# Performance work log

Hardware: AMD Instinct MI355X
Metric: run time of the kernel (lower is better)

The kernel has to match this reference:

```python
import jax, jax.numpy as jnp
import numpy as np

N = 50000      # nodes
E = 800000     # edges (avg degree 16)
D = 128        # hidden dim
L = 3          # message-passing layers
NU = 1         # DRew nu -> delay = max(k - nu, 0)


def setup_inputs() -> dict:
    key = jax.random.key(0)
    ks = jax.random.split(key, 6)
    x = jax.random.normal(ks[0], (N, D), dtype=jnp.float32)
    edge_index = jax.random.randint(ks[1], (2, E), 0, N)          # [2, E] (src, dst)
    edge_attr = jax.random.randint(ks[2], (E,), 1, L + 1)          # edge types in {1..L}
    scale = 1.0 / np.sqrt(D).astype(np.float32)
    Ws = jax.random.normal(ks[3], (L, D, D), dtype=jnp.float32) * scale       # mlp_s per layer
    bs = jnp.zeros((L, D), dtype=jnp.float32)
    Wk = jax.random.normal(ks[4], (L, L, D, D), dtype=jnp.float32) * scale    # mlp_k, padded; layer t uses k=1..t+1
    bk = jnp.zeros((L, L, D), dtype=jnp.float32)
    eps = jnp.zeros((L,), dtype=jnp.float32)
    return dict(x=x, edge_index=edge_index, edge_attr=edge_attr,
                Ws=Ws, bs=bs, Wk=Wk, bk=bk, eps=eps)


def reference(x, edge_index, edge_attr, Ws, bs, Wk, bk, eps):
    src, dst = edge_index[0], edge_index[1]
    xs = [x]
    for t in range(L):
        xt = xs[-1]
        # out = (1 + eps) * mlp_s(x)
        out = (1.0 + eps[t]) * jax.nn.relu(xt @ Ws[t] + bs[t])
        for k in range(1, t + 2):
            delay = max(k - NU, 0)
            x_src = xs[t - delay]                       # delayed node features
            mask = (edge_attr == k).astype(xt.dtype)    # edge-type mask (replaces boolean column select)
            msg = x_src[src] * mask[:, None]            # gather + mask: [E, D]
            agg = jax.ops.segment_sum(msg, dst, num_segments=N)  # scatter-add per destination
            out = out + jax.nn.relu(agg @ Wk[t, k - 1] + bk[t, k - 1])  # mlp_k(k)
        # gin_nn_post is an empty Sequential -> identity; then F.relu; then residual
        h = jax.nn.relu(out)
        xs.append(xt + h)
    return xs[-1]
```

## Files before the change

kernel.cpp:

```cpp
#include <hip/hip_runtime.h>
#include <hip/hip_bf16.h>


#define NODES 50000
#define EDGES 800000
#define DIM   128
#define ND    ((long)NODES * DIM)
#define NB3   (3 * NODES)
#define NPART 8
#define PSIZE (NODES / NPART)
#define NROWP 50048
#define NBLKS ((NB3 + 255) / 256)
#define NCELL 192
#define SORTN (NCELL * NBLKS)

typedef __attribute__((ext_vector_type(8))) short  bf16x8;
typedef __attribute__((ext_vector_type(4))) float  f32x4;

#define LDS_STRIDE 136

__global__ __launch_bounds__(256) void convw_kernel(
    const float* __restrict__ Ws, const float* __restrict__ Wk,
    __hip_bfloat16* __restrict__ WT) {
  int m = blockIdx.x;
  const float* src = (m < 3) ? (Ws + (long)m * 16384) : (Wk + (long)(m - 3) * 16384);
  __hip_bfloat16* dst = WT + (long)m * 16384;
  for (int idx = threadIdx.x; idx < 16384; idx += 256) {
    int k = idx >> 7, n = idx & 127;
    dst[n * 128 + k] = __float2bfloat16(src[idx]);
  }
}

__global__ __launch_bounds__(256) void x2b_kernel(
    const float4* __restrict__ xin, uint2* __restrict__ xbo, long n4) {
  long i = (long)blockIdx.x * 256 + threadIdx.x;
  if (i >= n4) return;
  float4 v = xin[i];
  union { __hip_bfloat16 h[4]; uint2 u; } pk;
  pk.h[0] = __float2bfloat16(v.x); pk.h[1] = __float2bfloat16(v.y);
  pk.h[2] = __float2bfloat16(v.z); pk.h[3] = __float2bfloat16(v.w);
  xbo[i] = pk.u;
}

__global__ __launch_bounds__(256) void zrow_kernel(
    __hip_bfloat16* __restrict__ xb0, __hip_bfloat16* __restrict__ xb1,
    __hip_bfloat16* __restrict__ xb2) {
  int i = threadIdx.x;
  if (i < DIM) {
    xb0[(long)NODES * DIM + i] = __float2bfloat16(0.f);
    xb1[(long)NODES * DIM + i] = __float2bfloat16(0.f);
    xb2[(long)NODES * DIM + i] = __float2bfloat16(0.f);
  }
}

__global__ __launch_bounds__(256) void hist_kernel(
    const int* __restrict__ ei, const int* __restrict__ attr,
    int* __restrict__ counts, int E) {
  int e = blockIdx.x * 256 + threadIdx.x;
  if (e >= E) return;
  atomicAdd(&counts[ei[E + e] * 3 + (attr[e] - 1)], 1);
}

__global__ __launch_bounds__(256) void scan_a_kernel(
    const int* __restrict__ counts, int* __restrict__ partial,
    int* __restrict__ blocksums, int n) {
  __shared__ int tmp[256];
  int gid = blockIdx.x * 256 + threadIdx.x;
  int v = (gid < n) ? ((counts[gid] + 3) & ~3) : 0;
  tmp[threadIdx.x] = v;
  __syncthreads();
  for (int off = 1; off < 256; off <<= 1) {
    int t = (threadIdx.x >= off) ? tmp[threadIdx.x - off] : 0;
    __syncthreads();
    tmp[threadIdx.x] += t;
    __syncthreads();
  }
  if (gid < n) partial[gid] = tmp[threadIdx.x] - v;
  if (threadIdx.x == 255) blocksums[blockIdx.x] = tmp[255];
}

__global__ __launch_bounds__(256) void scan_b_kernel(int* __restrict__ bs, int nb) {
  __shared__ int tmp[256];
  __shared__ int carry;
  if (threadIdx.x == 0) carry = 0;
  __syncthreads();
  for (int base = 0; base < nb; base += 256) {
    int gid = base + threadIdx.x;
    int v = (gid < nb) ? bs[gid] : 0;
    tmp[threadIdx.x] = v;
    __syncthreads();
    for (int off = 1; off < 256; off <<= 1) {
      int t = (threadIdx.x >= off) ? tmp[threadIdx.x - off] : 0;
      __syncthreads();
      tmp[threadIdx.x] += t;
      __syncthreads();
    }
    if (gid < nb) bs[gid] = tmp[threadIdx.x] - v + carry;
    __syncthreads();
    if (threadIdx.x == 0) carry += tmp[255];
    __syncthreads();
  }
}

__global__ __launch_bounds__(256) void scan_c_kernel(
    int* __restrict__ rowptr, int* __restrict__ cursor,
    const int* __restrict__ bs, int* __restrict__ csr, int n) {
  int gid = blockIdx.x * 256 + threadIdx.x;
  if (gid >= n) return;
  int cnt = cursor[gid];
  int pcnt = (cnt + 3) & ~3;
  int val = rowptr[gid] + bs[blockIdx.x];
  rowptr[gid] = val;
  cursor[gid] = val;
  for (int i = cnt; i < pcnt; ++i) csr[val + i] = NODES;
  if (gid == n - 1) rowptr[n] = val + pcnt;
}

__global__ __launch_bounds__(256) void fill_kernel(
    const int* __restrict__ ei, const int* __restrict__ attr,
    int* __restrict__ cursor, int* __restrict__ csr_src, int E) {
  int p = blockIdx.x & (NPART - 1);
  int chunk = blockIdx.x >> 3;
  int e = chunk * 256 + threadIdx.x;
  if (e >= E) return;
  int d = ei[E + e];
  int lo = p * PSIZE;
  if (d < lo || d >= lo + PSIZE) return;
  int pos = atomicAdd(&cursor[d * 3 + (attr[e] - 1)], 1);
  csr_src[pos] = ei[e];
}

__device__ __forceinline__ int bucket_cell(const int* rowptr, int b) {
  int c = (rowptr[b + 1] - rowptr[b]) >> 2;
  if (c > 63) c = 63;
  int km1 = b - (b / 3) * 3;
  return km1 * 64 + (63 - c);
}

__global__ __launch_bounds__(256) void bhist_kernel(
    const int* __restrict__ rowptr, int* __restrict__ G) {
  __shared__ int h[NCELL];
  if (threadIdx.x < NCELL) h[threadIdx.x] = 0;
  __syncthreads();
  int b = blockIdx.x * 256 + threadIdx.x;
  if (b < NB3) atomicAdd(&h[bucket_cell(rowptr, b)], 1);
  __syncthreads();
  if (threadIdx.x < NCELL) G[threadIdx.x * NBLKS + blockIdx.x] = h[threadIdx.x];
}

__global__ __launch_bounds__(256) void fscan_a_kernel(
    const int* __restrict__ in, int* __restrict__ partial,
    int* __restrict__ blocksums, int n) {
  __shared__ int tmp[256];
  int gid = blockIdx.x * 256 + threadIdx.x;
  int v = (gid < n) ? in[gid] : 0;
  tmp[threadIdx.x] = v;
  __syncthreads();
  for (int off = 1; off < 256; off <<= 1) {
    int t = (threadIdx.x >= off) ? tmp[threadIdx.x - off] : 0;
    __syncthreads();
    tmp[threadIdx.x] += t;
    __syncthreads();
  }
  if (gid < n) partial[gid] = tmp[threadIdx.x] - v;
  if (threadIdx.x == 255) blocksums[blockIdx.x] = tmp[255];
}

__global__ __launch_bounds__(256) void fscan_c_kernel(
    int* __restrict__ partial, const int* __restrict__ bs, int n) {
  int gid = blockIdx.x * 256 + threadIdx.x;
  if (gid >= n) return;
  partial[gid] += bs[blockIdx.x];
}

__global__ __launch_bounds__(256) void bfill_kernel(
    const int* __restrict__ rowptr, const int* __restrict__ Gscan,
    int* __restrict__ wl) {
  __shared__ int base[NCELL];
  if (threadIdx.x < NCELL)
    base[threadIdx.x] = Gscan[threadIdx.x * NBLKS + blockIdx.x];
  __syncthreads();
  int b = blockIdx.x * 256 + threadIdx.x;
  if (b >= NB3) return;
  int pos = atomicAdd(&base[bucket_cell(rowptr, b)], 1);
  wl[pos] = b;
}

__global__ __launch_bounds__(256, 6) void gather_kernel(
    const __hip_bfloat16* __restrict__ s0,
    const __hip_bfloat16* __restrict__ s1,
    const __hip_bfloat16* __restrict__ s2,
    const int* __restrict__ rowptr, const int* __restrict__ csr,
    const int* __restrict__ wl,
    __hip_bfloat16* __restrict__ ag0, __hip_bfloat16* __restrict__ ag1,
    __hip_bfloat16* __restrict__ ag2, int nwork) {
  int group = (blockIdx.x * 256 + threadIdx.x) >> 4;
  int lane16 = threadIdx.x & 15;
  if (group >= nwork) return;
  int b = wl[group];
  int d = b / 3;
  int km1 = b - d * 3;
  const __hip_bfloat16* xb = (km1 == 0) ? s0 : ((km1 == 1) ? s1 : s2);
  __hip_bfloat16* ag = (km1 == 0) ? ag0 : ((km1 == 1) ? ag1 : ag2);
  int beg = rowptr[b], end = rowptr[b + 1];
  float a0 = 0.f, a1 = 0.f, a2 = 0.f, a3 = 0.f,
        a4 = 0.f, a5 = 0.f, a6 = 0.f, a7 = 0.f;
  for (int base = beg; base < end; base += 16) {
    int idxv = csr[base + lane16];
    int cnt = end - base; if (cnt > 16) cnt = 16;
    for (int j = 0; j < cnt; j += 4) {
      int q0 = __shfl(idxv, j + 0, 16);
      int q1 = __shfl(idxv, j + 1, 16);
      int q2 = __shfl(idxv, j + 2, 16);
      int q3 = __shfl(idxv, j + 3, 16);
      uint4 v0 = *(const uint4*)(xb + (long)q0 * DIM + lane16 * 8);
      uint4 v1 = *(const uint4*)(xb + (long)q1 * DIM + lane16 * 8);
      uint4 v2 = *(const uint4*)(xb + (long)q2 * DIM + lane16 * 8);
      uint4 v3 = *(const uint4*)(xb + (long)q3 * DIM + lane16 * 8);
      a0 += __uint_as_float(v0.x << 16) + __uint_as_float(v1.x << 16)
          + __uint_as_float(v2.x << 16) + __uint_as_float(v3.x << 16);
      a1 += __uint_as_float(v0.x & 0xffff0000u) + __uint_as_float(v1.x & 0xffff0000u)
          + __uint_as_float(v2.x & 0xffff0000u) + __uint_as_float(v3.x & 0xffff0000u);
      a2 += __uint_as_float(v0.y << 16) + __uint_as_float(v1.y << 16)
          + __uint_as_float(v2.y << 16) + __uint_as_float(v3.y << 16);
      a3 += __uint_as_float(v0.y & 0xffff0000u) + __uint_as_float(v1.y & 0xffff0000u)
          + __uint_as_float(v2.y & 0xffff0000u) + __uint_as_float(v3.y & 0xffff0000u);
      a4 += __uint_as_float(v0.z << 16) + __uint_as_float(v1.z << 16)
          + __uint_as_float(v2.z << 16) + __uint_as_float(v3.z << 16);
      a5 += __uint_as_float(v0.z & 0xffff0000u) + __uint_as_float(v1.z & 0xffff0000u)
          + __uint_as_float(v2.z & 0xffff0000u) + __uint_as_float(v3.z & 0xffff0000u);
      a6 += __uint_as_float(v0.w << 16) + __uint_as_float(v1.w << 16)
          + __uint_as_float(v2.w << 16) + __uint_as_float(v3.w << 16);
      a7 += __uint_as_float(v0.w & 0xffff0000u) + __uint_as_float(v1.w & 0xffff0000u)
          + __uint_as_float(v2.w & 0xffff0000u) + __uint_as_float(v3.w & 0xffff0000u);
    }
  }
  union { __hip_bfloat16 h[8]; uint4 u; } pk;
  pk.h[0] = __float2bfloat16(a0); pk.h[1] = __float2bfloat16(a1);
  pk.h[2] = __float2bfloat16(a2); pk.h[3] = __float2bfloat16(a3);
  pk.h[4] = __float2bfloat16(a4); pk.h[5] = __float2bfloat16(a5);
  pk.h[6] = __float2bfloat16(a6); pk.h[7] = __float2bfloat16(a7);
  *(uint4*)(ag + (long)d * DIM + lane16 * 8) = pk.u;
}

__global__ __launch_bounds__(256, 4) void lgemm_kernel(
    const float* __restrict__ xt,
    const __hip_bfloat16* __restrict__ xbSelf,
    const __hip_bfloat16* __restrict__ ag0,
    const __hip_bfloat16* __restrict__ ag1,
    const __hip_bfloat16* __restrict__ ag2,
    const __hip_bfloat16* __restrict__ WT,
    const float* __restrict__ bs_t,
    const float* __restrict__ bk_t,
    const float* __restrict__ epsp,
    float* __restrict__ xn,
    __hip_bfloat16* __restrict__ xnb,
    int t) {
  __shared__ __hip_bfloat16 b_lds[128 * LDS_STRIDE];

  int tid = threadIdx.x;
  long row0 = (long)blockIdx.x * 64;
  int wave = tid >> 6, lane = tid & 63;
  int l15 = lane & 15, q = lane >> 4;
  long arow = row0 + wave * 16 + l15;

  const __hip_bfloat16* Asrc[4] = {xbSelf, ag0, ag1, ag2};
  f32x4 out[8];

  for (int p = 0; p <= t + 1; ++p) {
    if (p > 0) __syncthreads();
    const __hip_bfloat16* Am = Asrc[p];
    uint4 af[4];
#pragma unroll
    for (int k0i = 0; k0i < 4; ++k0i)
      af[k0i] = *(const uint4*)(Am + arow * DIM + k0i * 32 + 8 * q);
    const __hip_bfloat16* W = (p == 0) ? (WT + (long)t * 16384)
                                       : (WT + (long)(3 + t * 3 + (p - 1)) * 16384);
    {
      const uint4* bq = (const uint4*)W;
#pragma unroll
      for (int i = 0; i < 8; ++i) {
        int idx = tid + 256 * i;
        int n = idx >> 4, k8 = idx & 15;
        uint4 v = bq[idx];
        *(uint4*)(b_lds + n * LDS_STRIDE + k8 * 8) = v;
      }
    }
    __syncthreads();

    f32x4 acc[8] = {};
#pragma unroll
    for (int k0i = 0; k0i < 4; ++k0i) {
      bf16x8 a = __builtin_bit_cast(bf16x8, af[k0i]);
#pragma unroll
      for (int j = 0; j < 8; ++j) {
        bf16x8 bfr = *(const bf16x8*)(b_lds + (16 * j + l15) * LDS_STRIDE + k0i * 32 + 8 * q);
        acc[j] = __builtin_amdgcn_mfma_f32_16x16x32_bf16(a, bfr, acc[j], 0, 0, 0);
      }
    }
    if (p == 0) {
      float sc = 1.0f + *epsp;
#pragma unroll
      for (int j = 0; j < 8; ++j) {
        float b = bs_t[16 * j + l15];
#pragma unroll
        for (int r = 0; r < 4; ++r) out[j][r] = sc * fmaxf(acc[j][r] + b, 0.f);
      }
    } else {
      const float* bb = bk_t + (p - 1) * 128;
#pragma unroll
      for (int j = 0; j < 8; ++j) {
        float b = bb[16 * j + l15];
#pragma unroll
        for (int r = 0; r < 4; ++r) out[j][r] += fmaxf(acc[j][r] + b, 0.f);
      }
    }
  }

  long rbase = row0 + wave * 16 + q * 4;
#pragma unroll
  for (int j = 0; j < 8; ++j) {
    int col = 16 * j + l15;
#pragma unroll
    for (int r = 0; r < 4; ++r) {
      long grow = rbase + r;
      if (grow < NODES) {
        float v = xt[grow * DIM + col] + fmaxf(out[j][r], 0.f);
        xn[grow * DIM + col] = v;
        xnb[grow * DIM + col] = __float2bfloat16(v);
      }
    }
  }
}

extern "C" void kernel_launch(void* const* d_in, const int* in_sizes, int n_in,
                              void* d_out, int out_size, void* d_ws, size_t ws_size,
                              hipStream_t stream) {
  const float* x    = (const float*)d_in[0];
  const int*   ei   = (const int*)d_in[1];
  const int*   attr = (const int*)d_in[2];
  const float* Ws   = (const float*)d_in[3];
  const float* bs   = (const float*)d_in[4];
  const float* Wk   = (const float*)d_in[5];
  const float* bk   = (const float*)d_in[6];
  const float* eps  = (const float*)d_in[7];
  float* out = (float*)d_out;

  char* ws = (char*)d_ws;
  size_t off = 0;
  auto alloc = [&](size_t bytes) { char* p = ws + off; off += (bytes + 255) & ~(size_t)255; return p; };
  const size_t ROWB = (size_t)NROWP * DIM * 2;
  float* xs1 = (float*)alloc(ND * 4);
  float* xs2 = (float*)alloc(ND * 4);
  __hip_bfloat16* xb0 = (__hip_bfloat16*)alloc(ROWB);
  __hip_bfloat16* xb1 = (__hip_bfloat16*)alloc(ROWB);
  __hip_bfloat16* xb2 = (__hip_bfloat16*)alloc(ROWB);
  __hip_bfloat16* xb3 = (__hip_bfloat16*)alloc(ROWB);
  __hip_bfloat16* ag0 = (__hip_bfloat16*)alloc(ROWB);
  __hip_bfloat16* ag1 = (__hip_bfloat16*)alloc(ROWB);
  __hip_bfloat16* ag2 = (__hip_bfloat16*)alloc(ROWB);
  __hip_bfloat16* WT  = (__hip_bfloat16*)alloc(12 * 16384 * 2);
  int* cursor    = (int*)alloc((size_t)NB3 * 4);
  int* rowptr    = (int*)alloc((size_t)(NB3 + 1) * 4);
  int* blocksums = (int*)alloc(1024 * 4);
  int* G         = (int*)alloc((size_t)SORTN * 4);
  int* bsum2     = (int*)alloc(1024 * 4);
  int* wl        = (int*)alloc((size_t)NB3 * 4);
  int* csr_src   = (int*)alloc((size_t)(EDGES + 4 * NB3 + 16) * 4);

  hipLaunchKernelGGL(convw_kernel, dim3(12), dim3(256), 0, stream, Ws, Wk, WT);
  hipLaunchKernelGGL(x2b_kernel, dim3((int)(ND / 4 / 256)), dim3(256), 0, stream,
                     (const float4*)x, (uint2*)xb0, ND / 4);
  hipLaunchKernelGGL(zrow_kernel, dim3(1), dim3(256), 0, stream, xb0, xb1, xb2);
  hipMemsetAsync(cursor, 0, (size_t)NB3 * 4, stream);
  int egrid  = (EDGES + 255) / 256;
  int sgridA = (NB3 + 255) / 256;
  hipLaunchKernelGGL(hist_kernel, dim3(egrid), dim3(256), 0, stream, ei, attr, cursor, EDGES);
  hipLaunchKernelGGL(scan_a_kernel, dim3(sgridA), dim3(256), 0, stream, cursor, rowptr, blocksums, NB3);
  hipLaunchKernelGGL(scan_b_kernel, dim3(1), dim3(256), 0, stream, blocksums, sgridA);
  hipLaunchKernelGGL(scan_c_kernel, dim3(sgridA), dim3(256), 0, stream, rowptr, cursor, blocksums, csr_src, NB3);
  hipLaunchKernelGGL(fill_kernel, dim3(egrid * NPART), dim3(256), 0, stream, ei, attr, cursor, csr_src, EDGES);

  int fgrid = (SORTN + 255) / 256;
  hipLaunchKernelGGL(bhist_kernel, dim3(NBLKS), dim3(256), 0, stream, rowptr, G);
  hipLaunchKernelGGL(fscan_a_kernel, dim3(fgrid), dim3(256), 0, stream, G, G, bsum2, SORTN);
  hipLaunchKernelGGL(scan_b_kernel, dim3(1), dim3(256), 0, stream, bsum2, fgrid);
  hipLaunchKernelGGL(fscan_c_kernel, dim3(fgrid), dim3(256), 0, stream, G, bsum2, SORTN);
  hipLaunchKernelGGL(bfill_kernel, dim3(NBLKS), dim3(256), 0, stream, rowptr, G, wl);

  int ggrid = (NODES + 63) / 64;
  auto glaunch = [&](int nwork, const __hip_bfloat16* s0, const __hip_bfloat16* s1,
                     const __hip_bfloat16* s2) {
    int blocks = (nwork * 16 + 255) / 256;
    hipLaunchKernelGGL(gather_kernel, dim3(blocks), dim3(256), 0, stream,
                       s0, s1, s2, rowptr, csr_src, wl, ag0, ag1, ag2, nwork);
  };

  glaunch(NODES, xb0, nullptr, nullptr);
  hipLaunchKernelGGL(lgemm_kernel, dim3(ggrid), dim3(256), 0, stream,
                     x, xb0, ag0, ag1, ag2, WT, bs + 0, bk + 0, eps + 0, xs1, xb1, 0);
  glaunch(2 * NODES, xb1, xb0, nullptr);
  hipLaunchKernelGGL(lgemm_kernel, dim3(ggrid), dim3(256), 0, stream,
                     xs1, xb1, ag0, ag1, ag2, WT, bs + 128, bk + 3 * 128, eps + 1, xs2, xb2, 1);
  glaunch(3 * NODES, xb2, xb1, xb0);
  hipLaunchKernelGGL(lgemm_kernel, dim3(ggrid), dim3(256), 0, stream,
                     xs2, xb2, ag0, ag1, ag2, WT, bs + 256, bk + 6 * 128, eps + 2, out, xb3, 2);
}
```

Baseline: 358.5 us.

## Fuse setup kernels and keep residual stream in bf16 only

Merges weight conversion, x-to-bf16 conversion, zero-row writes and the cursor memset into one init kernel. Folds the bucket histogram into the scan-finalize kernel and the final scan add into bfill, cutting several launches. The lgemm epilogue now reads the residual from the bf16 copy and writes only bf16 for intermediate layers, writing fp32 only at the end. This drops fp32 residual reads and writes but accumulates the residual path in bf16, which loses precision.

```diff
diff --git a/kernel.cpp b/kernel.cpp
--- a/kernel.cpp
+++ b/kernel.cpp
@@ -19,37 +19,36 @@
 
 #define LDS_STRIDE 136
 
-__global__ __launch_bounds__(256) void convw_kernel(
-    const float* __restrict__ Ws, const float* __restrict__ Wk,
-    __hip_bfloat16* __restrict__ WT) {
-  int m = blockIdx.x;
-  const float* src = (m < 3) ? (Ws + (long)m * 16384) : (Wk + (long)(m - 3) * 16384);
-  __hip_bfloat16* dst = WT + (long)m * 16384;
-  for (int idx = threadIdx.x; idx < 16384; idx += 256) {
-    int k = idx >> 7, n = idx & 127;
-    dst[n * 128 + k] = __float2bfloat16(src[idx]);
-  }
-}
-
-__global__ __launch_bounds__(256) void x2b_kernel(
-    const float4* __restrict__ xin, uint2* __restrict__ xbo, long n4) {
-  long i = (long)blockIdx.x * 256 + threadIdx.x;
-  if (i >= n4) return;
-  float4 v = xin[i];
-  union { __hip_bfloat16 h[4]; uint2 u; } pk;
-  pk.h[0] = __float2bfloat16(v.x); pk.h[1] = __float2bfloat16(v.y);
-  pk.h[2] = __float2bfloat16(v.z); pk.h[3] = __float2bfloat16(v.w);
-  xbo[i] = pk.u;
-}
-
-__global__ __launch_bounds__(256) void zrow_kernel(
-    __hip_bfloat16* __restrict__ xb0, __hip_bfloat16* __restrict__ xb1,
-    __hip_bfloat16* __restrict__ xb2) {
-  int i = threadIdx.x;
-  if (i < DIM) {
-    xb0[(long)NODES * DIM + i] = __float2bfloat16(0.f);
-    xb1[(long)NODES * DIM + i] = __float2bfloat16(0.f);
-    xb2[(long)NODES * DIM + i] = __float2bfloat16(0.f);
+__global__ __launch_bounds__(256) void init_kernel(
+    const float* __restrict__ x, const float* __restrict__ Ws,
+    const float* __restrict__ Wk, __hip_bfloat16* __restrict__ xb0,
+    __hip_bfloat16* __restrict__ xb1, __hip_bfloat16* __restrict__ xb2,
+    __hip_bfloat16* __restrict__ WT, int* __restrict__ cursor) {
+  int b = blockIdx.x, tid = threadIdx.x;
+  long i = (long)b * 256 + tid;
+  if (i < ND / 4) {
+    float4 v = ((const float4*)x)[i];
+    union { __hip_bfloat16 h[4]; uint2 u; } pk;
+    pk.h[0] = __float2bfloat16(v.x); pk.h[1] = __float2bfloat16(v.y);
+    pk.h[2] = __float2bfloat16(v.z); pk.h[3] = __float2bfloat16(v.w);
+    ((uint2*)xb0)[i] = pk.u;
+  }
+  if (b < 12) {
+    const float* src = (b < 3) ? (Ws + (long)b * 16384) : (Wk + (long)(b - 3) * 16384);
+    __hip_bfloat16* dst = WT + (long)b * 16384;
+    for (int idx = tid; idx < 16384; idx += 256) {
+      int k = idx >> 7, n = idx & 127;
+      dst[n * 128 + k] = __float2bfloat16(src[idx]);
+    }
+  }
+  if (b >= 12 && b < 12 + NBLKS) {
+    int g = (b - 12) * 256 + tid;
+    if (g < NB3) cursor[g] = 0;
+  }
+  if (b == 599 && tid < DIM) {
+    xb0[(long)NODES * DIM + tid] = __float2bfloat16(0.f);
+    xb1[(long)NODES * DIM + tid] = __float2bfloat16(0.f);
+    xb2[(long)NODES * DIM + tid] = __float2bfloat16(0.f);
   }
 }
 
@@ -102,18 +101,28 @@
   }
 }
 
-__global__ __launch_bounds__(256) void scan_c_kernel(
+__global__ __launch_bounds__(256) void scanc_bhist_kernel(
     int* __restrict__ rowptr, int* __restrict__ cursor,
-    const int* __restrict__ bs, int* __restrict__ csr, int n) {
+    const int* __restrict__ bs, int* __restrict__ csr,
+    int* __restrict__ G, int n) {
+  __shared__ int h[NCELL];
+  if (threadIdx.x < NCELL) h[threadIdx.x] = 0;
+  __syncthreads();
   int gid = blockIdx.x * 256 + threadIdx.x;
-  if (gid >= n) return;
-  int cnt = cursor[gid];
-  int pcnt = (cnt + 3) & ~3;
-  int val = rowptr[gid] + bs[blockIdx.x];
-  rowptr[gid] = val;
-  cursor[gid] = val;
-  for (int i = cnt; i < pcnt; ++i) csr[val + i] = NODES;
-  if (gid == n - 1) rowptr[n] = val + pcnt;
+  if (gid < n) {
+    int cnt = cursor[gid];
+    int pcnt = (cnt + 3) & ~3;
+    int val = rowptr[gid] + bs[blockIdx.x];
+    rowptr[gid] = val;
+    cursor[gid] = val;
+    for (int i = cnt; i < pcnt; ++i) csr[val + i] = NODES;
+    if (gid == n - 1) rowptr[n] = val + pcnt;
+    int c = pcnt >> 2; if (c > 63) c = 63;
+    int km1 = gid - (gid / 3) * 3;
+    atomicAdd(&h[km1 * 64 + (63 - c)], 1);
+  }
+  __syncthreads();
+  if (threadIdx.x < NCELL) G[threadIdx.x * NBLKS + blockIdx.x] = h[threadIdx.x];
 }
 
 __global__ __launch_bounds__(256) void fill_kernel(
@@ -130,24 +139,6 @@
   csr_src[pos] = ei[e];
 }
 
-__device__ __forceinline__ int bucket_cell(const int* rowptr, int b) {
-  int c = (rowptr[b + 1] - rowptr[b]) >> 2;
-  if (c > 63) c = 63;
-  int km1 = b - (b / 3) * 3;
-  return km1 * 64 + (63 - c);
-}
-
-__global__ __launch_bounds__(256) void bhist_kernel(
-    const int* __restrict__ rowptr, int* __restrict__ G) {
-  __shared__ int h[NCELL];
-  if (threadIdx.x < NCELL) h[threadIdx.x] = 0;
-  __syncthreads();
-  int b = blockIdx.x * 256 + threadIdx.x;
-  if (b < NB3) atomicAdd(&h[bucket_cell(rowptr, b)], 1);
-  __syncthreads();
-  if (threadIdx.x < NCELL) G[threadIdx.x * NBLKS + blockIdx.x] = h[threadIdx.x];
-}
-
 __global__ __launch_bounds__(256) void fscan_a_kernel(
     const int* __restrict__ in, int* __restrict__ partial,
     int* __restrict__ blocksums, int n) {
@@ -166,23 +157,21 @@
   if (threadIdx.x == 255) blocksums[blockIdx.x] = tmp[255];
 }
 
-__global__ __launch_bounds__(256) void fscan_c_kernel(
-    int* __restrict__ partial, const int* __restrict__ bs, int n) {
-  int gid = blockIdx.x * 256 + threadIdx.x;
-  if (gid >= n) return;
-  partial[gid] += bs[blockIdx.x];
-}
-
 __global__ __launch_bounds__(256) void bfill_kernel(
-    const int* __restrict__ rowptr, const int* __restrict__ Gscan,
-    int* __restrict__ wl) {
+    const int* __restrict__ rowptr, const int* __restrict__ G,
+    const int* __restrict__ bsum2, int* __restrict__ wl) {
   __shared__ int base[NCELL];
-  if (threadIdx.x < NCELL)
-    base[threadIdx.x] = Gscan[threadIdx.x * NBLKS + blockIdx.x];
+  if (threadIdx.x < NCELL) {
+    int gidx = threadIdx.x * NBLKS + blockIdx.x;
+    base[threadIdx.x] = G[gidx] + bsum2[gidx >> 8];
+  }
   __syncthreads();
   int b = blockIdx.x * 256 + threadIdx.x;
   if (b >= NB3) return;
-  int pos = atomicAdd(&base[bucket_cell(rowptr, b)], 1);
+  int pcnt = rowptr[b + 1] - rowptr[b];
+  int c = pcnt >> 2; if (c > 63) c = 63;
+  int km1 = b - (b / 3) * 3;
+  int pos = atomicAdd(&base[km1 * 64 + (63 - c)], 1);
   wl[pos] = b;
 }
 
@@ -244,7 +233,6 @@
 }
 
 __global__ __launch_bounds__(256, 4) void lgemm_kernel(
-    const float* __restrict__ xt,
     const __hip_bfloat16* __restrict__ xbSelf,
     const __hip_bfloat16* __restrict__ ag0,
     const __hip_bfloat16* __restrict__ ag1,
@@ -253,8 +241,8 @@
     const float* __restrict__ bs_t,
     const float* __restrict__ bk_t,
     const float* __restrict__ epsp,
+    __hip_bfloat16* __restrict__ xnb,
     float* __restrict__ xn,
-    __hip_bfloat16* __restrict__ xnb,
     int t) {
   __shared__ __hip_bfloat16 b_lds[128 * LDS_STRIDE];
 
@@ -318,6 +306,7 @@
   }
 
   long rbase = row0 + wave * 16 + q * 4;
+  bool fin = (xn != nullptr);
 #pragma unroll
   for (int j = 0; j < 8; ++j) {
     int col = 16 * j + l15;
@@ -325,9 +314,10 @@
     for (int r = 0; r < 4; ++r) {
       long grow = rbase + r;
       if (grow < NODES) {
-        float v = xt[grow * DIM + col] + fmaxf(out[j][r], 0.f);
-        xn[grow * DIM + col] = v;
-        xnb[grow * DIM + col] = __float2bfloat16(v);
+        float res = __bfloat162float(xbSelf[grow * DIM + col]);
+        float v = res + fmaxf(out[j][r], 0.f);
+        if (fin) xn[grow * DIM + col] = v;
+        else     xnb[grow * DIM + col] = __float2bfloat16(v);
       }
     }
   }
@@ -350,12 +340,9 @@
   size_t off = 0;
   auto alloc = [&](size_t bytes) { char* p = ws + off; off += (bytes + 255) & ~(size_t)255; return p; };
   const size_t ROWB = (size_t)NROWP * DIM * 2;
-  float* xs1 = (float*)alloc(ND * 4);
-  float* xs2 = (float*)alloc(ND * 4);
   __hip_bfloat16* xb0 = (__hip_bfloat16*)alloc(ROWB);
   __hip_bfloat16* xb1 = (__hip_bfloat16*)alloc(ROWB);
   __hip_bfloat16* xb2 = (__hip_bfloat16*)alloc(ROWB);
-  __hip_bfloat16* xb3 = (__hip_bfloat16*)alloc(ROWB);
   __hip_bfloat16* ag0 = (__hip_bfloat16*)alloc(ROWB);
   __hip_bfloat16* ag1 = (__hip_bfloat16*)alloc(ROWB);
   __hip_bfloat16* ag2 = (__hip_bfloat16*)alloc(ROWB);
@@ -368,25 +355,21 @@
   int* wl        = (int*)alloc((size_t)NB3 * 4);
   int* csr_src   = (int*)alloc((size_t)(EDGES + 4 * NB3 + 16) * 4);
 
-  hipLaunchKernelGGL(convw_kernel, dim3(12), dim3(256), 0, stream, Ws, Wk, WT);
-  hipLaunchKernelGGL(x2b_kernel, dim3((int)(ND / 4 / 256)), dim3(256), 0, stream,
-                     (const float4*)x, (uint2*)xb0, ND / 4);
-  hipLaunchKernelGGL(zrow_kernel, dim3(1), dim3(256), 0, stream, xb0, xb1, xb2);
-  hipMemsetAsync(cursor, 0, (size_t)NB3 * 4, stream);
   int egrid  = (EDGES + 255) / 256;
-  int sgridA = (NB3 + 255) / 256;
+  int igrid  = (int)(ND / 4 / 256);
+  int fgrid  = (SORTN + 255) / 256;
+
+  hipLaunchKernelGGL(init_kernel, dim3(igrid), dim3(256), 0, stream,
+                     x, Ws, Wk, xb0, xb1, xb2, WT, cursor);
   hipLaunchKernelGGL(hist_kernel, dim3(egrid), dim3(256), 0, stream, ei, attr, cursor, EDGES);
-  hipLaunchKernelGGL(scan_a_kernel, dim3(sgridA), dim3(256), 0, stream, cursor, rowptr, blocksums, NB3);
-  hipLaunchKernelGGL(scan_b_kernel, dim3(1), dim3(256), 0, stream, blocksums, sgridA);
-  hipLaunchKernelGGL(scan_c_kernel, dim3(sgridA), dim3(256), 0, stream, rowptr, cursor, blocksums, csr_src, NB3);
+  hipLaunchKernelGGL(scan_a_kernel, dim3(NBLKS), dim3(256), 0, stream, cursor, rowptr, blocksums, NB3);
+  hipLaunchKernelGGL(scan_b_kernel, dim3(1), dim3(256), 0, stream, blocksums, NBLKS);
+  hipLaunchKernelGGL(scanc_bhist_kernel, dim3(NBLKS), dim3(256), 0, stream,
+                     rowptr, cursor, blocksums, csr_src, G, NB3);
   hipLaunchKernelGGL(fill_kernel, dim3(egrid * NPART), dim3(256), 0, stream, ei, attr, cursor, csr_src, EDGES);
-
-  int fgrid = (SORTN + 255) / 256;
-  hipLaunchKernelGGL(bhist_kernel, dim3(NBLKS), dim3(256), 0, stream, rowptr, G);
   hipLaunchKernelGGL(fscan_a_kernel, dim3(fgrid), dim3(256), 0, stream, G, G, bsum2, SORTN);
   hipLaunchKernelGGL(scan_b_kernel, dim3(1), dim3(256), 0, stream, bsum2, fgrid);
-  hipLaunchKernelGGL(fscan_c_kernel, dim3(fgrid), dim3(256), 0, stream, G, bsum2, SORTN);
-  hipLaunchKernelGGL(bfill_kernel, dim3(NBLKS), dim3(256), 0, stream, rowptr, G, wl);
+  hipLaunchKernelGGL(bfill_kernel, dim3(NBLKS), dim3(256), 0, stream, rowptr, G, bsum2, wl);
 
   int ggrid = (NODES + 63) / 64;
   auto glaunch = [&](int nwork, const __hip_bfloat16* s0, const __hip_bfloat16* s1,
@@ -398,11 +381,14 @@
 
   glaunch(NODES, xb0, nullptr, nullptr);
   hipLaunchKernelGGL(lgemm_kernel, dim3(ggrid), dim3(256), 0, stream,
-                     x, xb0, ag0, ag1, ag2, WT, bs + 0, bk + 0, eps + 0, xs1, xb1, 0);
+                     xb0, ag0, ag1, ag2, WT, bs + 0, bk + 0, eps + 0,
+                     xb1, (float*)nullptr, 0);
   glaunch(2 * NODES, xb1, xb0, nullptr);
   hipLaunchKernelGGL(lgemm_kernel, dim3(ggrid), dim3(256), 0, stream,
-                     xs1, xb1, ag0, ag1, ag2, WT, bs + 128, bk + 3 * 128, eps + 1, xs2, xb2, 1);
+                     xb1, ag0, ag1, ag2, WT, bs + 128, bk + 3 * 128, eps + 1,
+                     xb2, (float*)nullptr, 1);
   glaunch(3 * NODES, xb2, xb1, xb0);
   hipLaunchKernelGGL(lgemm_kernel, dim3(ggrid), dim3(256), 0, stream,
-                     xs2, xb2, ag0, ag1, ag2, WT, bs + 256, bk + 6 * 128, eps + 2, out, xb3, 2);
-}
+                     xb2, ag0, ag1, ag2, WT, bs + 256, bk + 6 * 128, eps + 2,
+                     (__hip_bfloat16*)nullptr, out, 2);
+}
```

Result: faster. 336.6 us (-6.1%).
